# Performance work log

Hardware: AMD Instinct MI355X
Metric: run time of the kernel (lower is better)

## Reference

```python
import jax, jax.numpy as jnp
import numpy as np

B, H, W, C = 32, 56, 56, 256
HEADS, WS, SS, MLP = 8, 7, 3, 1024
N = WS * WS          # tokens per window = 49
HD = C // HEADS      # head dim = 32
SCALE = HD ** -0.5
EPS = 1e-5


def _rel_pos_index():
    coords = np.stack(np.meshgrid(np.arange(WS), np.arange(WS), indexing='ij')).reshape(2, -1)
    rel = (coords[:, :, None] - coords[:, None, :]).transpose(1, 2, 0)
    rel[:, :, 0] += WS - 1
    rel[:, :, 1] += WS - 1
    rel[:, :, 0] *= 2 * WS - 1
    return rel.sum(-1)  # (49, 49) int


def _shift_mask():
    ma = np.zeros((H, W), np.float32)
    sl = (slice(0, -WS), slice(-WS, -SS), slice(-SS, None))
    cnt = 0
    for hs in sl:
        for ws_ in sl:
            ma[hs, ws_] = cnt
            cnt += 1
    mw = ma.reshape(H // WS, WS, W // WS, WS).transpose(0, 2, 1, 3).reshape(-1, N)
    diff = mw[:, None, :] - mw[:, :, None]
    return np.where(diff != 0, np.float32(-100.0), np.float32(0.0))  # (nW, 49, 49)


_RPI = _rel_pos_index()
_MASK = jnp.asarray(_shift_mask())


def _ln(x, g, b):
    mu = jnp.mean(x, -1, keepdims=True)
    var = jnp.mean(jnp.square(x - mu), -1, keepdims=True)
    return (x - mu) * jax.lax.rsqrt(var + EPS) * g + b


def setup_inputs() -> dict:
    key = jax.random.key(0)
    ks = jax.random.split(key, 6)
    s = 0.02
    return {
        'x': jax.random.normal(ks[0], (B, H * W, C), jnp.float32),
        'qkv_w': jax.random.normal(ks[1], (C, 3 * C), jnp.float32) * s,
        'qkv_b': jnp.zeros((3 * C,), jnp.float32),
        'proj_w': jax.random.normal(ks[2], (C, C), jnp.float32) * s,
        'proj_b': jnp.zeros((C,), jnp.float32),
        'rel_bias': jax.random.normal(ks[3], ((2 * WS - 1) ** 2, HEADS), jnp.float32) * s,
        'ln1_g': jnp.ones((C,), jnp.float32),
        'ln1_b': jnp.zeros((C,), jnp.float32),
        'ln2_g': jnp.ones((C,), jnp.float32),
        'ln2_b': jnp.zeros((C,), jnp.float32),
        'mlp_w1': jax.random.normal(ks[4], (C, MLP), jnp.float32) * s,
        'mlp_b1': jnp.zeros((MLP,), jnp.float32),
        'mlp_w2': jax.random.normal(ks[5], (MLP, C), jnp.float32) * s,
        'mlp_b2': jnp.zeros((C,), jnp.float32),
    }


def reference(x, qkv_w, qkv_b, proj_w, proj_b, rel_bias,
              ln1_g, ln1_b, ln2_g, ln2_b, mlp_w1, mlp_b1, mlp_w2, mlp_b2):
    b = x.shape[0]
    nW = (H // WS) * (W // WS)

    x_skip = x
    xn = _ln(x, ln1_g, ln1_b).reshape(b, H, W, C)
    shifted = jnp.roll(xn, (-SS, -SS), axis=(1, 2))
    # window partition -> (b*nW, N, C)
    xw = shifted.reshape(b, H // WS, WS, W // WS, WS, C)
    xw = xw.transpose(0, 1, 3, 2, 4, 5).reshape(-1, N, C)

    qkv = (xw @ qkv_w + qkv_b).reshape(-1, N, 3, HEADS, HD).transpose(2, 0, 3, 1, 4)
    q, k, v = qkv[0] * SCALE, qkv[1], qkv[2]  # (b*nW, heads, N, hd)

    attn = jnp.einsum('bhnd,bhmd->bhnm', q, k)
    bias = rel_bias[_RPI.reshape(-1)].reshape(N, N, HEADS).transpose(2, 0, 1)
    attn = attn + bias[None]
    attn = attn.reshape(b, nW, HEADS, N, N) + _MASK[None, :, None]
    attn = jax.nn.softmax(attn.reshape(-1, HEADS, N, N), axis=-1)

    out = jnp.einsum('bhnm,bhmd->bhnd', attn, v)
    out = out.transpose(0, 2, 1, 3).reshape(-1, N, C)
    out = out @ proj_w + proj_b

    # window reverse -> (b, H, W, C)
    out = out.reshape(b, H // WS, W // WS, WS, WS, C)
    out = out.transpose(0, 1, 3, 2, 4, 5).reshape(b, H, W, C)
    out = jnp.roll(out, (SS, SS), axis=(1, 2)).reshape(b, H * W, C)

    x = x_skip + out
    x_skip2 = x
    xn2 = _ln(x, ln2_g, ln2_b)
    h = jax.nn.gelu(xn2 @ mlp_w1 + mlp_b1, approximate=False)
    h = h @ mlp_w2 + mlp_b2
    return x_skip2 + h
```

## Files before the change

### kernel.cpp

```cpp
#include <hip/hip_runtime.h>


typedef unsigned short u16;
typedef __attribute__((ext_vector_type(8))) short bfrag8;
typedef __attribute__((ext_vector_type(8))) unsigned short u16x8;
typedef __attribute__((ext_vector_type(4))) float f32x4;

#define WS_TOK 49
#define C_DIM 256
#define M_ROWS 100352
#define N_WIN 2048
#define SCALE_Q 0.17677669529663689f

#if defined(__has_builtin)
#  if __has_builtin(__builtin_amdgcn_global_load_lds)
#    define HAVE_GLL 1
#  endif
#endif
#ifndef HAVE_GLL
#  define HAVE_GLL 0
#endif

__device__ __forceinline__ float u2f(u16 u) {
    union { unsigned int i; float f; } c; c.i = ((unsigned int)u) << 16; return c.f;
}
__device__ __forceinline__ u16 f2u(float f) {
    union { float f; unsigned int i; } c; c.f = f;
    unsigned int i = c.i;
    return (u16)((i + 0x7fffu + ((i >> 16) & 1u)) >> 16);
}
__device__ __forceinline__ int regionOf(int h) {
    return h < 49 ? 0 : (h < 53 ? 1 : 2);
}
__device__ __forceinline__ float gelu_tanh(float v) {
    const float y = 0.79788456080286536f * (v + 0.044715f * v * v * v);
    const float e = __expf(2.f * y);
    const float t = 1.f - 2.f / (e + 1.f);
    return 0.5f * v * (1.f + t);
}

__device__ __forceinline__ void g2l16(const u16* g, u16* l) {
#if HAVE_GLL
    __builtin_amdgcn_global_load_lds((const __attribute__((address_space(1))) void*)g,
                                     (__attribute__((address_space(3))) void*)l, 16, 0, 0);
#else
    *(bfrag8*)l = *(const bfrag8*)g;
#endif
}

__global__ void transpose_k(const float* __restrict__ in, u16* __restrict__ out,
                            int R, int Ccols) {
    int i = blockIdx.x * 256 + threadIdx.x;
    if (i < R * Ccols) {
        int r = i / Ccols, c = i - r * Ccols;
        out[(size_t)c * R + r] = f2u(in[i]);
    }
}

__global__ __launch_bounds__(256) void ln_kernel(const float* __restrict__ xin,
                                                 const float* __restrict__ g,
                                                 const float* __restrict__ b,
                                                 u16* __restrict__ out, int mode) {
    const int w = threadIdx.x >> 6, lane = threadIdx.x & 63;
    const int r = blockIdx.x * 4 + w;
    int s = r;
    if (mode == 0) {
        const int win = r / WS_TOK, tok = r - win * WS_TOK;
        const int b_ = win >> 6, w64 = win & 63;
        const int wr = w64 >> 3, wc = w64 & 7;
        const int th = tok / 7, tw = tok - th * 7;
        int hh = wr * 7 + th + 3; if (hh >= 56) hh -= 56;
        int ww = wc * 7 + tw + 3; if (ww >= 56) ww -= 56;
        s = b_ * 3136 + hh * 56 + ww;
    }
    const float4 u = *(const float4*)(xin + (size_t)s * C_DIM + lane * 4);
    float f0 = u.x, f1 = u.y, f2 = u.z, f3 = u.w;
    float s1 = f0 + f1 + f2 + f3;
    float s2 = f0 * f0 + f1 * f1 + f2 * f2 + f3 * f3;
#pragma unroll
    for (int off = 32; off; off >>= 1) {
        s1 += __shfl_xor(s1, off, 64);
        s2 += __shfl_xor(s2, off, 64);
    }
    const float mu = s1 * (1.f / 256.f);
    const float rs = rsqrtf(s2 * (1.f / 256.f) - mu * mu + 1e-5f);
    const float4 ug = *(const float4*)(g + lane * 4);
    const float4 ub = *(const float4*)(b + lane * 4);
    ushort4 o;
    o.x = f2u((f0 - mu) * rs * ug.x + ub.x);
    o.y = f2u((f1 - mu) * rs * ug.y + ub.y);
    o.z = f2u((f2 - mu) * rs * ug.z + ub.z);
    o.w = f2u((f3 - mu) * rs * ug.w + ub.w);
    *(ushort4*)(out + (size_t)r * C_DIM + lane * 4) = o;
}

template <int KD, int ND, int NY, int EPI>
__global__ __launch_bounds__(256) void gemm_bt(const u16* __restrict__ A,
                                               const u16* __restrict__ Bt,
                                               const float* __restrict__ bias,
                                               u16* __restrict__ o0,
                                               u16* __restrict__ o1,
                                               u16* __restrict__ o2,
                                               float* __restrict__ fo,
                                               const float* __restrict__ res) {
    __shared__ __align__(16) char pool[17408];
    u16* As = (u16*)pool;
    u16* Bs = (u16*)(pool + 8192);
    const int tid = threadIdx.x;
    const int bid = blockIdx.x;
    const int m0 = (bid / NY) * 128;
    const int n0 = (bid % NY) * 128;
    const int wid = tid >> 6, lane = tid & 63;
    const int wy = wid >> 1, wx = wid & 1;
    const int l15 = lane & 15, lsel = lane >> 4;

    f32x4 acc[4][4] = {};
    const u16* Ag = A + (size_t)m0 * KD;
    const u16* Bg = Bt + (size_t)n0 * KD;

    for (int k0 = 0; k0 < KD; k0 += 32) {
#pragma unroll
        for (int p = 0; p < 2; ++p) {
            const int idx = p * 256 + tid;
            const int row = idx >> 2, ks = (idx & 3) << 3;
            g2l16(Ag + (size_t)row * KD + k0 + ks, As + idx * 8);
            g2l16(Bg + (size_t)row * KD + k0 + ks, Bs + idx * 8);
        }
        __syncthreads();
        bfrag8 af[4], bfv[4];
#pragma unroll
        for (int m = 0; m < 4; ++m)
            af[m] = *(const bfrag8*)(As + (wy * 64 + m * 16 + l15) * 32 + lsel * 8);
#pragma unroll
        for (int n = 0; n < 4; ++n)
            bfv[n] = *(const bfrag8*)(Bs + (wx * 64 + n * 16 + l15) * 32 + lsel * 8);
#pragma unroll
        for (int m = 0; m < 4; ++m)
#pragma unroll
            for (int n = 0; n < 4; ++n)
                acc[m][n] = __builtin_amdgcn_mfma_f32_16x16x32_bf16(af[m], bfv[n],
                                                                    acc[m][n], 0, 0, 0);
        __syncthreads();
    }

    float* Ts = (float*)pool + wid * (16 * 68);
    const int r  = lane >> 2;
    const int cg = (lane & 3) << 4;

#pragma unroll
    for (int m = 0; m < 4; ++m) {
#pragma unroll
        for (int n = 0; n < 4; ++n)
#pragma unroll
            for (int reg = 0; reg < 4; ++reg)
                Ts[(lsel * 4 + reg) * 68 + n * 16 + l15] = acc[m][n][reg];
        float vals[16];
#pragma unroll
        for (int j = 0; j < 4; ++j)
            *(f32x4*)(vals + 4 * j) = *(const f32x4*)(Ts + r * 68 + cg + 4 * j);

        const int gr  = m0 + wy * 64 + m * 16 + r;
        const int gc0 = n0 + wx * 64 + cg;
        float bias16[16];
#pragma unroll
        for (int j = 0; j < 4; ++j)
            *(f32x4*)(bias16 + 4 * j) = *(const f32x4*)(bias + gc0 + 4 * j);

        if (EPI == 0) {
            const int win = gr / WS_TOK, tok = gr - win * WS_TOK;
            const int part = gc0 >> 8, head = (gc0 >> 5) & 7, hd = gc0 & 31;
            u16* dst = (part == 0) ? o0 : (part == 1) ? o1 : o2;
            const float sc = (part == 0) ? SCALE_Q : 1.f;
            const size_t di = (size_t)win * 8 * (WS_TOK * 32) + (size_t)tok * 32 +
                              (size_t)head * (WS_TOK * 32) + hd;
            u16x8 pk[2];
#pragma unroll
            for (int j = 0; j < 16; ++j)
                ((u16*)pk)[j] = f2u((vals[j] + bias16[j]) * sc);
            *(u16x8*)(dst + di)     = pk[0];
            *(u16x8*)(dst + di + 8) = pk[1];
        } else if (EPI == 1) {
            const int win = gr / WS_TOK, tok = gr - win * WS_TOK;
            const int b_ = win >> 6, w64 = win & 63;
            const int wr = w64 >> 3, wc = w64 & 7;
            const int th = tok / 7, tw = tok - th * 7;
            int hh = wr * 7 + th + 3; if (hh >= 56) hh -= 56;
            int ww = wc * 7 + tw + 3; if (ww >= 56) ww -= 56;
            const size_t di = ((size_t)b_ * 3136 + hh * 56 + ww) * C_DIM + gc0;
#pragma unroll
            for (int j = 0; j < 4; ++j) {
                f32x4 rr = *(const f32x4*)(res + di + 4 * j);
                f32x4 o;
#pragma unroll
                for (int e = 0; e < 4; ++e)
                    o[e] = rr[e] + vals[4 * j + e] + bias16[4 * j + e];
                *(f32x4*)(fo + di + 4 * j) = o;
            }
        } else if (EPI == 2) {
            u16x8 pk[2];
#pragma unroll
            for (int j = 0; j < 16; ++j)
                ((u16*)pk)[j] = f2u(gelu_tanh(vals[j] + bias16[j]));
            u16* dst = o0 + (size_t)gr * ND + gc0;
            *(u16x8*)dst       = pk[0];
            *(u16x8*)(dst + 8) = pk[1];
        } else {
            const size_t di = (size_t)gr * ND + gc0;
#pragma unroll
            for (int j = 0; j < 4; ++j) {
                f32x4 rr = *(const f32x4*)(res + di + 4 * j);
                f32x4 o;
#pragma unroll
                for (int e = 0; e < 4; ++e)
                    o[e] = rr[e] + vals[4 * j + e] + bias16[4 * j + e];
                *(f32x4*)(fo + di + 4 * j) = o;
            }
        }
    }
}

__global__ __launch_bounds__(256, 2) void fused_mlp(const u16* __restrict__ z,
                                                    const u16* __restrict__ w1T,
                                                    const float* __restrict__ b1,
                                                    const u16* __restrict__ w2T,
                                                    const float* __restrict__ b2,
                                                    float* __restrict__ out) {
    __shared__ __align__(16) u16 pool[20480];
    u16* sA  = pool;
    u16* sB1 = pool + 4096;
    u16* sB2 = pool;
    u16* hc  = pool + 12288;
    const int tid = threadIdx.x;
    const int wid = tid >> 6, lane = tid & 63;
    const int wy = wid >> 1, wx = wid & 1;
    const int l15 = lane & 15, lsel = lane >> 4;
    const int m0 = blockIdx.x * 64;

    f32x4 acc2[2][8] = {};

    for (int kc = 0; kc < 8; ++kc) {
        f32x4 acc1[2][4] = {};
        const u16* w1c = w1T + ((size_t)kc << 7) * 256;
        for (int k0 = 0; k0 < 256; k0 += 64) {
#pragma unroll
            for (int p = 0; p < 2; ++p) {
                const int i = p * 256 + tid;
                const int row = i >> 3, s = i & 7;
                g2l16(z + (size_t)(m0 + row) * 256 + k0 + ((s ^ (row & 7)) << 3),
                      sA + i * 8);
            }
#pragma unroll
            for (int p = 0; p < 4; ++p) {
                const int i = p * 256 + tid;
                const int row = i >> 3, s = i & 7;
                g2l16(w1c + (size_t)row * 256 + k0 + ((s ^ (row & 7)) << 3),
                      sB1 + i * 8);
            }
            __syncthreads();
#pragma unroll
            for (int sub = 0; sub < 2; ++sub) {
                bfrag8 af[2], bf[4];
#pragma unroll
                for (int m = 0; m < 2; ++m) {
                    const int r = wy * 32 + m * 16 + l15;
                    af[m] = *(const bfrag8*)(sA + r * 64 +
                             ((sub * 32 + lsel * 8) ^ ((r & 7) << 3)));
                }
#pragma unroll
                for (int n = 0; n < 4; ++n) {
                    const int r = wx * 64 + n * 16 + l15;
                    bf[n] = *(const bfrag8*)(sB1 + r * 64 +
                             ((sub * 32 + lsel * 8) ^ ((r & 7) << 3)));
                }
#pragma unroll
                for (int m = 0; m < 2; ++m)
#pragma unroll
                    for (int n = 0; n < 4; ++n)
                        acc1[m][n] = __builtin_amdgcn_mfma_f32_16x16x32_bf16(
                            af[m], bf[n], acc1[m][n], 0, 0, 0);
            }
            __syncthreads();
        }
        float b1v[4];
#pragma unroll
        for (int n = 0; n < 4; ++n)
            b1v[n] = b1[(kc << 7) + wx * 64 + n * 16 + l15];
#pragma unroll
        for (int m = 0; m < 2; ++m)
#pragma unroll
            for (int n = 0; n < 4; ++n)
#pragma unroll
                for (int reg = 0; reg < 4; ++reg) {
                    const int rh = wy * 32 + m * 16 + lsel * 4 + reg;
                    const int ch = wx * 64 + n * 16 + l15;
                    hc[rh * 128 + (ch ^ ((rh & 15) << 3))] =
                        f2u(gelu_tanh(acc1[m][n][reg] + b1v[n]));
                }

        for (int ks = 0; ks < 4; ++ks) {
#pragma unroll
            for (int p = 0; p < 4; ++p) {
                const int i = p * 256 + tid;
                const int n = i >> 2, s = i & 3;
                g2l16(w2T + (size_t)n * 1024 + (kc << 7) + ks * 32 +
                          ((s ^ ((n >> 1) & 3)) << 3),
                      sB2 + i * 8);
            }
            __syncthreads();
            bfrag8 a2[2], bb[8];
#pragma unroll
            for (int m = 0; m < 2; ++m) {
                const int r = wy * 32 + m * 16 + l15;
                a2[m] = *(const bfrag8*)(hc + r * 128 +
                         ((ks * 32 + lsel * 8) ^ ((r & 15) << 3)));
            }
#pragma unroll
            for (int n = 0; n < 8; ++n) {
                const int r = wx * 128 + n * 16 + l15;
                bb[n] = *(const bfrag8*)(sB2 + r * 32 +
                         ((lsel * 8) ^ (((r >> 1) & 3) << 3)));
            }
#pragma unroll
            for (int m = 0; m < 2; ++m)
#pragma unroll
                for (int n = 0; n < 8; ++n)
                    acc2[m][n] = __builtin_amdgcn_mfma_f32_16x16x32_bf16(
                        a2[m], bb[n], acc2[m][n], 0, 0, 0);
            __syncthreads();
        }
    }

    float b2v[8];
#pragma unroll
    for (int n = 0; n < 8; ++n)
        b2v[n] = b2[wx * 128 + n * 16 + l15];
#pragma unroll
    for (int m = 0; m < 2; ++m)
#pragma unroll
        for (int reg = 0; reg < 4; ++reg) {
            const int row = m0 + wy * 32 + m * 16 + lsel * 4 + reg;
#pragma unroll
            for (int n = 0; n < 8; ++n) {
                const size_t di = (size_t)row * 256 + wx * 128 + n * 16 + l15;
                out[di] += acc2[m][n][reg] + b2v[n];
            }
        }
}

__global__ __launch_bounds__(256) void attn_kernel(const u16* __restrict__ q,
                                                   const u16* __restrict__ k,
                                                   const u16* __restrict__ v,
                                                   const float* __restrict__ relb,
                                                   u16* __restrict__ ao) {
    __shared__ __align__(16) u16 PbAll[4][64 * 64];
    __shared__ __align__(16) u16 VtAll[4][32 * 64];
    const int wid = threadIdx.x >> 6;
    const int lane = threadIdx.x & 63;
    u16* Pb = PbAll[wid];
    u16* Vt = VtAll[wid];
    const int bid = blockIdx.x * 4 + wid;
    const int head = bid & 7, win = bid >> 3;
    const int w64 = win & 63;
    const int wr = w64 >> 3, wc = w64 & 7;
    const int l15 = lane & 15, lsel = lane >> 4;
    const size_t base = (size_t)bid * (WS_TOK * 32);
    const u16* qb = q + base;
    const u16* kb = k + base;
    const u16* vb = v + base;

    for (int idx = lane; idx < WS_TOK * 32; idx += 64) {
        const int tok = idx >> 5, dim = idx & 31;
        Vt[dim * 64 + tok] = vb[idx];
    }
    for (int i = lane; i < 32 * 15; i += 64) {
        const int dim = i / 15, tok = 49 + (i - dim * 15);
        Vt[dim * 64 + tok] = 0;
    }

    bfrag8 qf[4], kf[4];
#pragma unroll
    for (int m = 0; m < 4; ++m) {
        int tok = m * 16 + l15; if (tok > 48) tok = 48;
        qf[m] = *(const bfrag8*)(qb + tok * 32 + lsel * 8);
    }
#pragma unroll
    for (int n = 0; n < 4; ++n) {
        int tok = n * 16 + l15; if (tok > 48) tok = 48;
        kf[n] = *(const bfrag8*)(kb + tok * 32 + lsel * 8);
    }
    f32x4 S[4][4] = {};
#pragma unroll
    for (int m = 0; m < 4; ++m)
#pragma unroll
        for (int n = 0; n < 4; ++n)
            S[m][n] = __builtin_amdgcn_mfma_f32_16x16x32_bf16(qf[m], kf[n], S[m][n], 0, 0, 0);

#pragma unroll
    for (int m = 0; m < 4; ++m) {
#pragma unroll
        for (int reg = 0; reg < 4; ++reg) {
            const int row = m * 16 + lsel * 4 + reg;
            const int rowc = row > 48 ? 48 : row;
            const int ih = rowc / 7, iw = rowc - ih * 7;
            const int ri = regionOf(wr * 7 + ih) * 3 + regionOf(wc * 7 + iw);
            float sv[4];
#pragma unroll
            for (int n = 0; n < 4; ++n) {
                const int col = n * 16 + l15;
                float val = S[m][n][reg];
                if (col > 48) {
                    val = -1e30f;
                } else {
                    const int jh = col / 7, jw = col - jh * 7;
                    val += relb[((ih - jh + 6) * 13 + (iw - jw + 6)) * 8 + head];
                    const int rj = regionOf(wr * 7 + jh) * 3 + regionOf(wc * 7 + jw);
                    if (ri != rj) val -= 100.f;
                }
                sv[n] = val;
            }
            float mx = fmaxf(fmaxf(sv[0], sv[1]), fmaxf(sv[2], sv[3]));
#pragma unroll
            for (int off = 1; off < 16; off <<= 1) mx = fmaxf(mx, __shfl_xor(mx, off, 64));
            float p[4], sum = 0.f;
#pragma unroll
            for (int n = 0; n < 4; ++n) { p[n] = __expf(sv[n] - mx); sum += p[n]; }
#pragma unroll
            for (int off = 1; off < 16; off <<= 1) sum += __shfl_xor(sum, off, 64);
            const float inv = 1.f / sum;
#pragma unroll
            for (int n = 0; n < 4; ++n)
                Pb[row * 64 + n * 16 + l15] = f2u(p[n] * inv);
        }
    }

    f32x4 O[4][2] = {};
    bfrag8 vf[2][2];
#pragma unroll
    for (int n = 0; n < 2; ++n) {
        vf[n][0] = *(const bfrag8*)(Vt + (n * 16 + l15) * 64 + lsel * 8);
        vf[n][1] = *(const bfrag8*)(Vt + (n * 16 + l15) * 64 + 32 + lsel * 8);
    }
#pragma unroll
    for (int m = 0; m < 4; ++m) {
        const bfrag8 pf0 = *(const bfrag8*)(Pb + (m * 16 + l15) * 64 + lsel * 8);
        const bfrag8 pf1 = *(const bfrag8*)(Pb + (m * 16 + l15) * 64 + 32 + lsel * 8);
#pragma unroll
        for (int n = 0; n < 2; ++n) {
            O[m][n] = __builtin_amdgcn_mfma_f32_16x16x32_bf16(pf0, vf[n][0], O[m][n], 0, 0, 0);
            O[m][n] = __builtin_amdgcn_mfma_f32_16x16x32_bf16(pf1, vf[n][1], O[m][n], 0, 0, 0);
        }
    }
    const size_t aob = (size_t)win * (WS_TOK * C_DIM) + head * 32;
#pragma unroll
    for (int m = 0; m < 4; ++m) {
#pragma unroll
        for (int reg = 0; reg < 4; ++reg) {
            const int row = m * 16 + lsel * 4 + reg;
            if (row < WS_TOK) {
#pragma unroll
                for (int n = 0; n < 2; ++n)
                    ao[aob + (size_t)row * C_DIM + n * 16 + l15] = f2u(O[m][n][reg]);
            }
        }
    }
}

extern "C" void kernel_launch(void* const* d_in, const int* in_sizes, int n_in,
                              void* d_out, int out_size, void* d_ws, size_t ws_size,
                              hipStream_t stream) {
    (void)in_sizes; (void)n_in; (void)out_size; (void)ws_size;
    const float* x      = (const float*)d_in[0];
    const float* qkv_w  = (const float*)d_in[1];
    const float* qkv_b  = (const float*)d_in[2];
    const float* proj_w = (const float*)d_in[3];
    const float* proj_b = (const float*)d_in[4];
    const float* relb   = (const float*)d_in[5];
    const float* ln1g   = (const float*)d_in[6];
    const float* ln1b   = (const float*)d_in[7];
    const float* ln2g   = (const float*)d_in[8];
    const float* ln2b   = (const float*)d_in[9];
    const float* w1     = (const float*)d_in[10];
    const float* b1     = (const float*)d_in[11];
    const float* w2     = (const float*)d_in[12];
    const float* b2     = (const float*)d_in[13];
    float* out = (float*)d_out;

    const size_t SZ = (size_t)M_ROWS * C_DIM;
    u16* wsu  = (u16*)d_ws;
    u16* xw   = wsu;
    u16* qq   = wsu + SZ;
    u16* kk   = wsu + 2 * SZ;
    u16* vv   = wsu + 3 * SZ;
    u16* ao   = wsu + 4 * SZ;
    u16* z    = xw;
    u16* qkvT = wsu + 5 * SZ;
    u16* projT = qkvT + 256 * 768;
    u16* w1T  = projT + 256 * 256;
    u16* w2T  = w1T + 256 * 1024;

    transpose_k<<<768, 256, 0, stream>>>(qkv_w, qkvT, 256, 768);
    transpose_k<<<256, 256, 0, stream>>>(proj_w, projT, 256, 256);
    transpose_k<<<1024, 256, 0, stream>>>(w1, w1T, 256, 1024);
    transpose_k<<<1024, 256, 0, stream>>>(w2, w2T, 1024, 256);

    ln_kernel<<<M_ROWS / 4, 256, 0, stream>>>(x, ln1g, ln1b, xw, 0);

    gemm_bt<256, 768, 6, 0><<<784 * 6, 256, 0, stream>>>(xw, qkvT, qkv_b,
                                                         qq, kk, vv, nullptr, nullptr);

    attn_kernel<<<N_WIN * 8 / 4, 256, 0, stream>>>(qq, kk, vv, relb, ao);

    gemm_bt<256, 256, 2, 1><<<784 * 2, 256, 0, stream>>>(ao, projT, proj_b,
                                                         nullptr, nullptr, nullptr, out, x);

    ln_kernel<<<M_ROWS / 4, 256, 0, stream>>>(out, ln2g, ln2b, z, 1);

    fused_mlp<<<M_ROWS / 64, 256, 0, stream>>>(z, w1T, b1, w2T, b2, out);
}
```

Before: 768.4 us.

## Double-buffer MLP weight tiles and keep the full activation tile resident in LDS

The fused MLP kernel now loads the whole 64x256 input activation tile into LDS once, instead of reloading it for every hidden chunk. It ping-pongs two weight buffers so the next W1 or W2 tile is prefetched while MFMAs run on the current one, crossing the phase boundary between the two GEMMs. This cuts one barrier per stage and hides global-load latency. LDS use doubles to 80KB per block, which may lower occupancy below the two blocks the launch bounds request.

```diff
diff --git a/kernel.cpp b/kernel.cpp
--- a/kernel.cpp
+++ b/kernel.cpp
@@ -219,57 +219,82 @@
     }
 }
 
+__device__ __forceinline__ void stage_w1t(const u16* __restrict__ w1T, u16* dst,
+                                          int kc, int k0, int tid) {
+#pragma unroll
+    for (int p = 0; p < 4; ++p) {
+        const int i = p * 256 + tid;
+        const int row = i >> 3, s = i & 7;
+        g2l16(w1T + (size_t)(kc * 128 + row) * 256 + k0 + ((s ^ (row & 7)) << 3),
+              dst + i * 8);
+    }
+}
+__device__ __forceinline__ void stage_w2t(const u16* __restrict__ w2T, u16* dst,
+                                          int kc, int bs, int tid) {
+#pragma unroll
+    for (int p = 0; p < 4; ++p) {
+        const int i = p * 256 + tid;
+        const int row = i >> 2, s = i & 3;
+        g2l16(w2T + (size_t)row * 1024 + kc * 128 + bs * 32 +
+                  ((s ^ ((row >> 1) & 3)) << 3),
+              dst + i * 8);
+    }
+}
+
 __global__ __launch_bounds__(256, 2) void fused_mlp(const u16* __restrict__ z,
                                                     const u16* __restrict__ w1T,
                                                     const float* __restrict__ b1,
                                                     const u16* __restrict__ w2T,
                                                     const float* __restrict__ b2,
                                                     float* __restrict__ out) {
-    __shared__ __align__(16) u16 pool[20480];
-    u16* sA  = pool;
-    u16* sB1 = pool + 4096;
-    u16* sB2 = pool;
-    u16* hc  = pool + 12288;
+    __shared__ __align__(16) u16 pool[40960];
+    u16* zS  = pool;
+    u16* wb0 = pool + 16384;
+    u16* wb1 = pool + 24576;
+    u16* hc  = pool + 32768;
     const int tid = threadIdx.x;
     const int wid = tid >> 6, lane = tid & 63;
     const int wy = wid >> 1, wx = wid & 1;
     const int l15 = lane & 15, lsel = lane >> 4;
     const int m0 = blockIdx.x * 64;
 
+#pragma unroll
+    for (int p = 0; p < 8; ++p) {
+        const int i = p * 256 + tid;
+        const int row = i >> 5, s = i & 31;
+        g2l16(z + (size_t)(m0 + row) * 256 + ((s ^ (row & 7)) << 3), zS + i * 8);
+    }
+    stage_w1t(w1T, wb0, 0, 0, tid);
+    __syncthreads();
+
     f32x4 acc2[2][8] = {};
 
     for (int kc = 0; kc < 8; ++kc) {
+        float b1v[4];
+#pragma unroll
+        for (int n = 0; n < 4; ++n)
+            b1v[n] = b1[kc * 128 + wx * 64 + n * 16 + l15];
+
         f32x4 acc1[2][4] = {};
-        const u16* w1c = w1T + ((size_t)kc << 7) * 256;
-        for (int k0 = 0; k0 < 256; k0 += 64) {
-#pragma unroll
-            for (int p = 0; p < 2; ++p) {
-                const int i = p * 256 + tid;
-                const int row = i >> 3, s = i & 7;
-                g2l16(z + (size_t)(m0 + row) * 256 + k0 + ((s ^ (row & 7)) << 3),
-                      sA + i * 8);
-            }
-#pragma unroll
-            for (int p = 0; p < 4; ++p) {
-                const int i = p * 256 + tid;
-                const int row = i >> 3, s = i & 7;
-                g2l16(w1c + (size_t)row * 256 + k0 + ((s ^ (row & 7)) << 3),
-                      sB1 + i * 8);
-            }
-            __syncthreads();
+#pragma unroll
+        for (int ks = 0; ks < 4; ++ks) {
+            u16* wc = (ks & 1) ? wb1 : wb0;
+            u16* wn = (ks & 1) ? wb0 : wb1;
+            if (ks < 3) stage_w1t(w1T, wn, kc, (ks + 1) * 64, tid);
+            else        stage_w2t(w2T, wn, kc, 0, tid);
 #pragma unroll
             for (int sub = 0; sub < 2; ++sub) {
                 bfrag8 af[2], bf[4];
 #pragma unroll
                 for (int m = 0; m < 2; ++m) {
                     const int r = wy * 32 + m * 16 + l15;
-                    af[m] = *(const bfrag8*)(sA + r * 64 +
-                             ((sub * 32 + lsel * 8) ^ ((r & 7) << 3)));
+                    af[m] = *(const bfrag8*)(zS + r * 256 +
+                             ((ks * 64 + sub * 32 + lsel * 8) ^ ((r & 7) << 3)));
                 }
 #pragma unroll
                 for (int n = 0; n < 4; ++n) {
                     const int r = wx * 64 + n * 16 + l15;
-                    bf[n] = *(const bfrag8*)(sB1 + r * 64 +
+                    bf[n] = *(const bfrag8*)(wc + r * 64 +
                              ((sub * 32 + lsel * 8) ^ ((r & 7) << 3)));
                 }
 #pragma unroll
@@ -279,45 +304,38 @@
                         acc1[m][n] = __builtin_amdgcn_mfma_f32_16x16x32_bf16(
                             af[m], bf[n], acc1[m][n], 0, 0, 0);
             }
+            if (ks == 3) {
+#pragma unroll
+                for (int m = 0; m < 2; ++m)
+#pragma unroll
+                    for (int n = 0; n < 4; ++n)
+#pragma unroll
+                        for (int reg = 0; reg < 4; ++reg) {
+                            const int rh = wy * 32 + m * 16 + lsel * 4 + reg;
+                            const int ch = wx * 64 + n * 16 + l15;
+                            hc[rh * 128 + (ch ^ ((rh & 15) << 3))] =
+                                f2u(gelu_tanh(acc1[m][n][reg] + b1v[n]));
+                        }
+            }
             __syncthreads();
         }
-        float b1v[4];
-#pragma unroll
-        for (int n = 0; n < 4; ++n)
-            b1v[n] = b1[(kc << 7) + wx * 64 + n * 16 + l15];
-#pragma unroll
-        for (int m = 0; m < 2; ++m)
-#pragma unroll
-            for (int n = 0; n < 4; ++n)
-#pragma unroll
-                for (int reg = 0; reg < 4; ++reg) {
-                    const int rh = wy * 32 + m * 16 + lsel * 4 + reg;
-                    const int ch = wx * 64 + n * 16 + l15;
-                    hc[rh * 128 + (ch ^ ((rh & 15) << 3))] =
-                        f2u(gelu_tanh(acc1[m][n][reg] + b1v[n]));
-                }
-
-        for (int ks = 0; ks < 4; ++ks) {
-#pragma unroll
-            for (int p = 0; p < 4; ++p) {
-                const int i = p * 256 + tid;
-                const int n = i >> 2, s = i & 3;
-                g2l16(w2T + (size_t)n * 1024 + (kc << 7) + ks * 32 +
-                          ((s ^ ((n >> 1) & 3)) << 3),
-                      sB2 + i * 8);
-            }
-            __syncthreads();
+#pragma unroll
+        for (int bs = 0; bs < 4; ++bs) {
+            u16* wc = (bs & 1) ? wb1 : wb0;
+            u16* wn = (bs & 1) ? wb0 : wb1;
+            if (bs < 3)      stage_w2t(w2T, wn, kc, bs + 1, tid);
+            else if (kc < 7) stage_w1t(w1T, wn, kc + 1, 0, tid);
             bfrag8 a2[2], bb[8];
 #pragma unroll
             for (int m = 0; m < 2; ++m) {
                 const int r = wy * 32 + m * 16 + l15;
                 a2[m] = *(const bfrag8*)(hc + r * 128 +
-                         ((ks * 32 + lsel * 8) ^ ((r & 15) << 3)));
+                         ((bs * 32 + lsel * 8) ^ ((r & 15) << 3)));
             }
 #pragma unroll
             for (int n = 0; n < 8; ++n) {
                 const int r = wx * 128 + n * 16 + l15;
-                bb[n] = *(const bfrag8*)(sB2 + r * 32 +
+                bb[n] = *(const bfrag8*)(wc + r * 32 +
                          ((lsel * 8) ^ (((r >> 1) & 3) << 3)));
             }
 #pragma unroll
```

New measurement: 717.4 us. -6.6%, faster.
